# Kernel optimization log

Hardware: AMD Instinct MI355X
Metric: run time of the kernel (lower is better)

Reference implementation:

```python
import jax, jax.numpy as jnp
import numpy as np

CE_WEIGHT = 1.0
TRIPLET_WEIGHT = 0.1
MARGIN = 0.2


def setup_inputs() -> dict:
    key = jax.random.key(0)
    k1, k2, k3 = jax.random.split(key, 3)
    B, D, V = 4096, 512, 6000
    logits = jax.random.normal(k1, (B, V), dtype=jnp.float32)
    embeddings = jax.random.normal(k2, (B, D), dtype=jnp.float32)
    labels = jax.random.randint(k3, (B,), 0, 512, dtype=jnp.int64)
    return {"logits": logits, "embeddings": embeddings, "labels": labels}


def _pairwise_dist(emb):
    # Euclidean cdist via gram matrix; safe sqrt (zero grad where d2 == 0).
    sq = jnp.sum(emb * emb, axis=-1)  # [B]
    d2 = sq[:, None] + sq[None, :] - 2.0 * (emb @ emb.T)  # [B, B]
    d2 = jnp.maximum(d2, 0.0)
    safe = jnp.where(d2 > 0.0, d2, 1.0)
    return jnp.where(d2 > 0.0, jnp.sqrt(safe), 0.0)


def _losses(logits, embeddings, labels):
    B = logits.shape[0]
    # Cross entropy (mean reduction, matching nn.CrossEntropyLoss).
    logp = jax.nn.log_softmax(logits, axis=-1)
    ce_loss = -jnp.mean(jnp.take_along_axis(logp, labels[:, None], axis=1)[:, 0])

    # Batch-hard triplet loss, fully vectorized (one masked amax/amin per row).
    dist = _pairwise_dist(embeddings)  # [B, B]
    same = labels[:, None] == labels[None, :]  # [B, B]
    eye = jnp.eye(B, dtype=bool)
    pos_mask = same & ~eye
    neg_mask = ~same
    neg_inf = jnp.float32(-np.inf)
    pos_inf = jnp.float32(np.inf)
    hardest_pos = jnp.max(jnp.where(pos_mask, dist, neg_inf), axis=1)  # [B]
    hardest_neg = jnp.min(jnp.where(neg_mask, dist, pos_inf), axis=1)  # [B]
    valid = jnp.any(pos_mask, axis=1) & jnp.any(neg_mask, axis=1)  # [B]
    per_row = jax.nn.relu(hardest_pos - hardest_neg + MARGIN)
    per_row = jnp.where(valid, per_row, 0.0)
    n_valid = jnp.sum(valid.astype(jnp.float32))
    triplet_loss = jnp.where(n_valid > 0, jnp.sum(per_row) / jnp.maximum(n_valid, 1.0), 0.0)

    total_loss = CE_WEIGHT * ce_loss + TRIPLET_WEIGHT * triplet_loss
    return total_loss, ce_loss, triplet_loss


def reference(logits, embeddings, labels):
    return _losses(logits, embeddings, labels)
```

## Files before the change

### kernel.cpp

```cpp
#include <hip/hip_runtime.h>
#include <hip/hip_bf16.h>
#include <math.h>

#define BN   4096
#define DN   512
#define VN   6000
#define NCLS 512

typedef __attribute__((ext_vector_type(8)))  short short8;
typedef __attribute__((ext_vector_type(16))) float f32x16;

__device__ __forceinline__ unsigned short f2bf(float x) {
  unsigned int u = __float_as_uint(x);
  u = (u + 0x7FFFu + ((u >> 16) & 1u)) >> 16;
  return (unsigned short)u;
}

__device__ __forceinline__ void gld_lds16(const unsigned short* g, unsigned short* l) {
  __builtin_amdgcn_global_load_lds(
      (const __attribute__((address_space(1))) void*)g,
      (__attribute__((address_space(3))) void*)l, 16, 0, 0);
}

__launch_bounds__(128)
__global__ void prep_kernel(const float* __restrict__ emb, const int* __restrict__ labels,
                            unsigned short* __restrict__ embh, float* __restrict__ sqn,
                            int* __restrict__ cnt, int* __restrict__ posb,
                            int* __restrict__ negb) {
  int row = blockIdx.x;
  int tid = threadIdx.x;
  const float4* rp = (const float4*)(emb + (size_t)row * DN);
  float4 v = rp[tid];
  float ss = v.x * v.x + v.y * v.y + v.z * v.z + v.w * v.w;
  ushort4 h;
  h.x = f2bf(v.x); h.y = f2bf(v.y); h.z = f2bf(v.z); h.w = f2bf(v.w);
  ((ushort4*)(embh + (size_t)row * DN))[tid] = h;
#pragma unroll
  for (int off = 1; off < 64; off <<= 1) ss += __shfl_xor(ss, off);
  __shared__ float parts[2];
  if ((tid & 63) == 0) parts[tid >> 6] = ss;
  __syncthreads();
  if (tid == 0) {
    sqn[row] = parts[0] + parts[1];
    posb[row] = 0;
    negb[row] = 0x7F800000;
    atomicAdd(cnt + labels[row], 1);
  }
}

__launch_bounds__(256)
__global__ void ce_kernel(const float* __restrict__ logits,
                          const int* __restrict__ labels,
                          float* __restrict__ ce_part) {
  const int row = blockIdx.x;
  const float* rp = logits + (size_t)row * VN;
  const int tid = threadIdx.x;
  const int lab = labels[row];
  const float xlab = rp[lab];
  const float4* rp4 = (const float4*)rp;
  float4 v[6];
#pragma unroll
  for (int u = 0; u < 6; ++u) {
    int j = tid + u * 256;
    if (j < VN / 4) v[u] = rp4[j];
  }
  float s = 0.f;
#pragma unroll
  for (int u = 0; u < 6; ++u) {
    int j = tid + u * 256;
    if (j < VN / 4)
      s += __expf(v[u].x) + __expf(v[u].y) + __expf(v[u].z) + __expf(v[u].w);
  }
#pragma unroll
  for (int off = 1; off < 64; off <<= 1) s += __shfl_xor(s, off);
  __shared__ float sp[4];
  if ((tid & 63) == 0) sp[tid >> 6] = s;
  __syncthreads();
  if (tid == 0) {
    float S = sp[0] + sp[1] + sp[2] + sp[3];
    ce_part[row] = logf(S) - xlab;
  }
}

__launch_bounds__(64, 2)
__global__ void triplet_kernel(const unsigned short* __restrict__ embh,
                               const float* __restrict__ sqn,
                               const int* __restrict__ labels,
                               int* __restrict__ posb, int* __restrict__ negb) {
  __shared__ unsigned short sA[64 * 64];
  __shared__ unsigned short sB[64 * 64];

  const int lane = threadIdx.x;
  const int m = lane & 31;
  const int half = lane >> 5;

  const int t = blockIdx.x;
  int J = (int)((sqrtf(8.f * (float)t + 1.f) - 1.f) * 0.5f);
  while ((J + 1) * (J + 2) / 2 <= t) ++J;
  while (J * (J + 1) / 2 > t) --J;
  const int I = t - J * (J + 1) / 2;
  const int i0 = I * 64, j0 = J * 64;
  const bool diag = (I == J);

  const int lrow = lane >> 3;
  const int lchk = (lane & 7) ^ lrow;
  const unsigned short* gA = embh + (size_t)(i0 + lrow) * DN + lchk * 8;
  const unsigned short* gB = embh + (size_t)(j0 + lrow) * DN + lchk * 8;

  f32x16 acc[2][2] = {};
  f32x16 accT[2][2] = {};

  for (int ks = 0; ks < 8; ++ks) {
    const int kk = ks * 64;
    asm volatile("s_waitcnt lgkmcnt(0)" ::: "memory");
#pragma unroll
    for (int s = 0; s < 8; ++s)
      gld_lds16(gA + kk + (size_t)s * 8 * DN, &sA[s * 8 * 64]);
#pragma unroll
    for (int s = 0; s < 8; ++s)
      gld_lds16(gB + kk + (size_t)s * 8 * DN, &sB[s * 8 * 64]);
    asm volatile("s_waitcnt vmcnt(0)" ::: "memory");
#pragma unroll
    for (int q = 0; q < 4; ++q) {
      const int c = q * 2 + half;
      const int sw = ((c ^ (m & 7)) * 8);
      short8 a0 = *(const short8*)&sA[m * 64 + sw];
      short8 a1 = *(const short8*)&sA[(32 + m) * 64 + sw];
      short8 b0 = *(const short8*)&sB[m * 64 + sw];
      short8 b1 = *(const short8*)&sB[(32 + m) * 64 + sw];
      acc[0][0]  = __builtin_amdgcn_mfma_f32_32x32x16_bf16(a0, b0, acc[0][0], 0, 0, 0);
      acc[0][1]  = __builtin_amdgcn_mfma_f32_32x32x16_bf16(a0, b1, acc[0][1], 0, 0, 0);
      acc[1][0]  = __builtin_amdgcn_mfma_f32_32x32x16_bf16(a1, b0, acc[1][0], 0, 0, 0);
      acc[1][1]  = __builtin_amdgcn_mfma_f32_32x32x16_bf16(a1, b1, acc[1][1], 0, 0, 0);
      accT[0][0] = __builtin_amdgcn_mfma_f32_32x32x16_bf16(b0, a0, accT[0][0], 0, 0, 0);
      accT[0][1] = __builtin_amdgcn_mfma_f32_32x32x16_bf16(b0, a1, accT[0][1], 0, 0, 0);
      accT[1][0] = __builtin_amdgcn_mfma_f32_32x32x16_bf16(b1, a0, accT[1][0], 0, 0, 0);
      accT[1][1] = __builtin_amdgcn_mfma_f32_32x32x16_bf16(b1, a1, accT[1][1], 0, 0, 0);
    }
  }

  {
    const int gj0 = j0 + m, gj1 = j0 + 32 + m;
    const int cl0 = labels[gj0], cl1 = labels[gj1];
    const float cq0 = sqn[gj0], cq1 = sqn[gj1];
    float p0 = 0.f, p1 = 0.f, n0 = INFINITY, n1 = INFINITY;
#pragma unroll
    for (int rb = 0; rb < 2; ++rb) {
#pragma unroll
      for (int r = 0; r < 16; ++r) {
        const int gi = i0 + rb * 32 + (r & 3) + 8 * (r >> 2) + 4 * half;
        const int rl = labels[gi];
        const float rq = sqn[gi];
        const float d0 = fmaf(-2.f, acc[rb][0][r], rq + cq0);
        const float d1 = fmaf(-2.f, acc[rb][1][r], rq + cq1);
        if (rl == cl0) { if (gi != gj0) p0 = fmaxf(p0, d0); } else n0 = fminf(n0, d0);
        if (rl == cl1) { if (gi != gj1) p1 = fmaxf(p1, d1); } else n1 = fminf(n1, d1);
      }
    }
    p0 = fmaxf(p0, __shfl_xor(p0, 32)); n0 = fminf(n0, __shfl_xor(n0, 32));
    p1 = fmaxf(p1, __shfl_xor(p1, 32)); n1 = fminf(n1, __shfl_xor(n1, 32));
    if (half == 0) {
      atomicMax(posb + gj0, __float_as_int(p0));
      atomicMin(negb + gj0, __float_as_int(n0));
      atomicMax(posb + gj1, __float_as_int(p1));
      atomicMin(negb + gj1, __float_as_int(n1));
    }
  }

  if (!diag) {
    const int gj0 = i0 + m, gj1 = i0 + 32 + m;
    const int cl0 = labels[gj0], cl1 = labels[gj1];
    const float cq0 = sqn[gj0], cq1 = sqn[gj1];
    float p0 = 0.f, p1 = 0.f, n0 = INFINITY, n1 = INFINITY;
#pragma unroll
    for (int rb = 0; rb < 2; ++rb) {
#pragma unroll
      for (int r = 0; r < 16; ++r) {
        const int gi = j0 + rb * 32 + (r & 3) + 8 * (r >> 2) + 4 * half;
        const int rl = labels[gi];
        const float rq = sqn[gi];
        const float d0 = fmaf(-2.f, accT[rb][0][r], rq + cq0);
        const float d1 = fmaf(-2.f, accT[rb][1][r], rq + cq1);
        if (rl == cl0) p0 = fmaxf(p0, d0); else n0 = fminf(n0, d0);
        if (rl == cl1) p1 = fmaxf(p1, d1); else n1 = fminf(n1, d1);
      }
    }
    p0 = fmaxf(p0, __shfl_xor(p0, 32)); n0 = fminf(n0, __shfl_xor(n0, 32));
    p1 = fmaxf(p1, __shfl_xor(p1, 32)); n1 = fminf(n1, __shfl_xor(n1, 32));
    if (half == 0) {
      atomicMax(posb + gj0, __float_as_int(p0));
      atomicMin(negb + gj0, __float_as_int(n0));
      atomicMax(posb + gj1, __float_as_int(p1));
      atomicMin(negb + gj1, __float_as_int(n1));
    }
  }
}

__launch_bounds__(1024)
__global__ void finalize_kernel(const int* __restrict__ posb, const int* __restrict__ negb,
                                const int* __restrict__ labels, const int* __restrict__ cnt,
                                const float* __restrict__ ce_part, float* __restrict__ out) {
  const int tid = threadIdx.x;
  float cesum = 0.f, sum = 0.f, nv = 0.f;
#pragma unroll
  for (int u = 0; u < 4; ++u) {
    const int i = tid + u * 1024;
    cesum += ce_part[i];
    int c = cnt[labels[i]];
    float p = sqrtf(fmaxf(__int_as_float(posb[i]), 0.f));
    float n = sqrtf(fmaxf(__int_as_float(negb[i]), 0.f));
    float t = fmaxf(p - n + 0.2f, 0.f);
    if (c >= 2 && c < BN) { sum += t; nv += 1.f; }
  }
#pragma unroll
  for (int off = 1; off < 64; off <<= 1) {
    cesum += __shfl_xor(cesum, off);
    sum   += __shfl_xor(sum, off);
    nv    += __shfl_xor(nv, off);
  }
  __shared__ float s0[16], s1[16], s2[16];
  if ((tid & 63) == 0) { s0[tid >> 6] = cesum; s1[tid >> 6] = sum; s2[tid >> 6] = nv; }
  __syncthreads();
  if (tid == 0) {
    cesum = 0.f; sum = 0.f; nv = 0.f;
#pragma unroll
    for (int wv = 0; wv < 16; ++wv) { cesum += s0[wv]; sum += s1[wv]; nv += s2[wv]; }
    float trip = (nv > 0.f) ? sum / nv : 0.f;
    float ce = cesum * (1.f / BN);
    out[0] = ce + 0.1f * trip;
    out[1] = ce;
    out[2] = trip;
  }
}

extern "C" void kernel_launch(void* const* d_in, const int* in_sizes, int n_in,
                              void* d_out, int out_size, void* d_ws, size_t ws_size,
                              hipStream_t stream) {
  const float* logits = (const float*)d_in[0];
  const float* emb    = (const float*)d_in[1];
  const int*   labels = (const int*)d_in[2];
  float* out = (float*)d_out;

  char* ws = (char*)d_ws;
  unsigned short* embh = (unsigned short*)ws;
  float* sqn    = (float*)(ws + (size_t)BN * DN * 2);
  int*   posb   = (int*)((char*)sqn  + (size_t)BN * 4);
  int*   negb   = (int*)((char*)posb + (size_t)BN * 4);
  int*   cnt    = (int*)((char*)negb + (size_t)BN * 4);
  float* ce_part = (float*)((char*)cnt + (size_t)NCLS * 4);

  hipMemsetAsync(cnt, 0, (size_t)NCLS * 4, stream);
  hipLaunchKernelGGL(prep_kernel, dim3(BN), dim3(128), 0, stream,
                     emb, labels, embh, sqn, cnt, posb, negb);
  hipLaunchKernelGGL(ce_kernel, dim3(BN), dim3(256), 0, stream,
                     logits, labels, ce_part);
  hipLaunchKernelGGL(triplet_kernel, dim3(64 * 65 / 2), dim3(64), 0, stream,
                     embh, sqn, labels, posb, negb);
  hipLaunchKernelGGL(finalize_kernel, dim3(1), dim3(1024), 0, stream,
                     posb, negb, labels, cnt, ce_part, out);
}
```

Measured before the change: 191.9 us.

## Fuse CE and triplet kernels into one interleaved launch for overlap

The separate cross-entropy and triplet kernels are merged into one kernel with 256-thread blocks. Blocks are interleaved so that each group of nine blocks runs one block of four triplet tiles (one per wave) and eight CE rows. The aim is to overlap the memory-bound logits reduction with the MFMA-bound distance tiles and to drop one launch. The risks are lower occupancy from 64KB of shared memory per block and imbalance between the two block types.

```diff
diff --git a/kernel.cpp b/kernel.cpp
--- a/kernel.cpp
+++ b/kernel.cpp
@@ -6,6 +6,7 @@
 #define DN   512
 #define VN   6000
 #define NCLS 512
+#define TJOBS 2080
 
 typedef __attribute__((ext_vector_type(8)))  short short8;
 typedef __attribute__((ext_vector_type(16))) float f32x16;
@@ -48,53 +49,15 @@
   }
 }
 
-__launch_bounds__(256)
-__global__ void ce_kernel(const float* __restrict__ logits,
-                          const int* __restrict__ labels,
-                          float* __restrict__ ce_part) {
-  const int row = blockIdx.x;
-  const float* rp = logits + (size_t)row * VN;
-  const int tid = threadIdx.x;
-  const int lab = labels[row];
-  const float xlab = rp[lab];
-  const float4* rp4 = (const float4*)rp;
-  float4 v[6];
-#pragma unroll
-  for (int u = 0; u < 6; ++u) {
-    int j = tid + u * 256;
-    if (j < VN / 4) v[u] = rp4[j];
-  }
-  float s = 0.f;
-#pragma unroll
-  for (int u = 0; u < 6; ++u) {
-    int j = tid + u * 256;
-    if (j < VN / 4)
-      s += __expf(v[u].x) + __expf(v[u].y) + __expf(v[u].z) + __expf(v[u].w);
-  }
-#pragma unroll
-  for (int off = 1; off < 64; off <<= 1) s += __shfl_xor(s, off);
-  __shared__ float sp[4];
-  if ((tid & 63) == 0) sp[tid >> 6] = s;
-  __syncthreads();
-  if (tid == 0) {
-    float S = sp[0] + sp[1] + sp[2] + sp[3];
-    ce_part[row] = logf(S) - xlab;
-  }
-}
-
-__launch_bounds__(64, 2)
-__global__ void triplet_kernel(const unsigned short* __restrict__ embh,
-                               const float* __restrict__ sqn,
-                               const int* __restrict__ labels,
-                               int* __restrict__ posb, int* __restrict__ negb) {
-  __shared__ unsigned short sA[64 * 64];
-  __shared__ unsigned short sB[64 * 64];
-
-  const int lane = threadIdx.x;
+__device__ __forceinline__ void triplet_job(int t, unsigned short* sA, unsigned short* sB,
+                                            const unsigned short* __restrict__ embh,
+                                            const float* __restrict__ sqn,
+                                            const int* __restrict__ labels,
+                                            int* __restrict__ posb,
+                                            int* __restrict__ negb, int lane) {
   const int m = lane & 31;
   const int half = lane >> 5;
 
-  const int t = blockIdx.x;
   int J = (int)((sqrtf(8.f * (float)t + 1.f) - 1.f) * 0.5f);
   while ((J + 1) * (J + 2) / 2 <= t) ++J;
   while (J * (J + 1) / 2 > t) --J;
@@ -196,6 +159,66 @@
   }
 }
 
+__launch_bounds__(256, 2)
+__global__ void fused_kernel(const float* __restrict__ logits,
+                             const int* __restrict__ labels,
+                             float* __restrict__ ce_part,
+                             const unsigned short* __restrict__ embh,
+                             const float* __restrict__ sqn,
+                             int* __restrict__ posb, int* __restrict__ negb) {
+  __shared__ unsigned short smem[4 * 8192];
+  const int b = blockIdx.x;
+  const int tid = threadIdx.x;
+  const int wave = tid >> 6;
+  const int lane = tid & 63;
+
+  int trip_job = -1;
+  int ce_row = -1;
+  if (b < 8) {
+    trip_job = 2048 + b * 4 + wave;
+  } else {
+    const int g = b - 8;
+    const int grp = g / 9;
+    const int pos = g - grp * 9;
+    if (pos == 0) trip_job = grp * 4 + wave;
+    else          ce_row = grp * 8 + pos - 1;
+  }
+
+  if (trip_job >= 0) {
+    unsigned short* sA = smem + wave * 8192;
+    unsigned short* sB = sA + 4096;
+    triplet_job(trip_job, sA, sB, embh, sqn, labels, posb, negb, lane);
+    return;
+  }
+
+  const float* rp = logits + (size_t)ce_row * VN;
+  const int lab = labels[ce_row];
+  const float xlab = rp[lab];
+  const float4* rp4 = (const float4*)rp;
+  float4 v[6];
+#pragma unroll
+  for (int u = 0; u < 6; ++u) {
+    int j = tid + u * 256;
+    if (j < VN / 4) v[u] = rp4[j];
+  }
+  float s = 0.f;
+#pragma unroll
+  for (int u = 0; u < 6; ++u) {
+    int j = tid + u * 256;
+    if (j < VN / 4)
+      s += __expf(v[u].x) + __expf(v[u].y) + __expf(v[u].z) + __expf(v[u].w);
+  }
+#pragma unroll
+  for (int off = 1; off < 64; off <<= 1) s += __shfl_xor(s, off);
+  float* sp = (float*)smem;
+  if (lane == 0) sp[wave] = s;
+  __syncthreads();
+  if (tid == 0) {
+    float S = sp[0] + sp[1] + sp[2] + sp[3];
+    ce_part[ce_row] = logf(S) - xlab;
+  }
+}
+
 __launch_bounds__(1024)
 __global__ void finalize_kernel(const int* __restrict__ posb, const int* __restrict__ negb,
                                 const int* __restrict__ labels, const int* __restrict__ cnt,
@@ -252,10 +275,8 @@
   hipMemsetAsync(cnt, 0, (size_t)NCLS * 4, stream);
   hipLaunchKernelGGL(prep_kernel, dim3(BN), dim3(128), 0, stream,
                      emb, labels, embh, sqn, cnt, posb, negb);
-  hipLaunchKernelGGL(ce_kernel, dim3(BN), dim3(256), 0, stream,
-                     logits, labels, ce_part);
-  hipLaunchKernelGGL(triplet_kernel, dim3(64 * 65 / 2), dim3(64), 0, stream,
-                     embh, sqn, labels, posb, negb);
+  hipLaunchKernelGGL(fused_kernel, dim3(8 + 512 * 9), dim3(256), 0, stream,
+                     logits, labels, ce_part, embh, sqn, posb, negb);
   hipLaunchKernelGGL(finalize_kernel, dim3(1), dim3(1024), 0, stream,
                      posb, negb, labels, cnt, ce_part, out);
 }
```

Result: slower. 199.1 us (+3.7%).
